# Optimization experiments

Hardware: AMD Instinct MI355X
Metric: run time of the kernel (lower is better)

Reference implementation:

```python
import jax, jax.numpy as jnp
import numpy as np

# dims
M, C, D = 64, 2000, 512          # clients, classes, embed_dim
H = 4                             # num_heads
HD = D // H                       # head_dim = 128
DFF = 2048                        # torch TransformerEncoderLayer default dim_feedforward
NUM_CLASSES = 2000
EPS = 1e-5


def _ln(x, g, b):
    mu = jnp.mean(x, axis=-1, keepdims=True)
    var = jnp.mean(jnp.square(x - mu), axis=-1, keepdims=True)
    return (x - mu) * jax.lax.rsqrt(var + EPS) * g + b


def setup_inputs() -> dict:
    key = jax.random.key(0)
    ks = jax.random.split(key, 16)
    s = 0.02
    return {
        "client_protos": jax.random.normal(ks[0], (M, C, D), jnp.float32),
        "norm_g": jnp.ones((D,), jnp.float32),
        "norm_b": jnp.zeros((D,), jnp.float32),
        "in_proj_w": jax.random.normal(ks[1], (3 * D, D), jnp.float32) * s,
        "in_proj_b": jnp.zeros((3 * D,), jnp.float32),
        "out_proj_w": jax.random.normal(ks[2], (D, D), jnp.float32) * s,
        "out_proj_b": jnp.zeros((D,), jnp.float32),
        "lin1_w": jax.random.normal(ks[3], (DFF, D), jnp.float32) * s,
        "lin1_b": jnp.zeros((DFF,), jnp.float32),
        "lin2_w": jax.random.normal(ks[4], (D, DFF), jnp.float32) * s,
        "lin2_b": jnp.zeros((D,), jnp.float32),
        "norm1_g": jnp.ones((D,), jnp.float32),
        "norm1_b": jnp.zeros((D,), jnp.float32),
        "norm2_g": jnp.ones((D,), jnp.float32),
        "norm2_b": jnp.zeros((D,), jnp.float32),
        "global_query": jax.random.normal(ks[5], (NUM_CLASSES, D), jnp.float32),
        "all_labels": jax.random.randint(ks[6], (C,), 0, NUM_CLASSES, jnp.int32),
        "round_num": 10,
        "client_idx": 0,
    }


def reference(client_protos, norm_g, norm_b, in_proj_w, in_proj_b,
              out_proj_w, out_proj_b, lin1_w, lin1_b, lin2_w, lin2_b,
              norm1_g, norm1_b, norm2_g, norm2_b, global_query,
              all_labels, round_num, client_idx):
    # 1) LayerNorm over all prototypes: (M, C, D)
    x = _ln(client_protos, norm_g, norm_b)
    # 2) Per-class transformer: original loops c in range(C) on (1, M, D).
    #    Batched: treat C as batch -> (C, M, D). Post-norm torch encoder layer.
    x = jnp.transpose(x, (1, 0, 2))  # (C, M, D)
    # self-attention
    qkv = x @ in_proj_w.T + in_proj_b          # (C, M, 3D)
    q, k, v = jnp.split(qkv, 3, axis=-1)
    q = q.reshape(C, M, H, HD)
    k = k.reshape(C, M, H, HD)
    v = v.reshape(C, M, H, HD)
    scores = jnp.einsum('cqhd,ckhd->chqk', q, k) / np.sqrt(HD).astype(np.float32)
    attn = jax.nn.softmax(scores, axis=-1)
    sa = jnp.einsum('chqk,ckhd->cqhd', attn, v).reshape(C, M, D)
    sa = sa @ out_proj_w.T + out_proj_b
    x = _ln(x + sa, norm1_g, norm1_b)
    # feed-forward (relu, dropout = eval no-op)
    ff = jax.nn.relu(x @ lin1_w.T + lin1_b) @ lin2_w.T + lin2_b
    x = _ln(x + ff, norm2_g, norm2_b)           # (C, M, D) == protos_trans^T
    # 3) Cross-attention with per-class global query
    q_all = global_query[all_labels].reshape(C, H, HD)
    kv_all = x.reshape(C, M, H, HD)
    s2 = jnp.einsum('chd,cmhd->chm', q_all, kv_all) / np.sqrt(HD).astype(np.float32)
    w2 = jax.nn.softmax(s2, axis=-1)
    attn_out = jnp.einsum('chm,cmhd->chd', w2, kv_all).reshape(C, D)
    return attn_out
```

## Files before the change

### kernel.cpp

```cpp
#include <hip/hip_runtime.h>

typedef _Float16 f16;
typedef _Float16 half4 __attribute__((ext_vector_type(4)));
typedef _Float16 half8 __attribute__((ext_vector_type(8)));
typedef float f32x4 __attribute__((ext_vector_type(4)));

typedef __attribute__((address_space(1))) void* as1v;
typedef __attribute__((address_space(3))) void* as3v;

#define SCALE 0.08838834764831845f

static __device__ __forceinline__ f32x4 mfma16(half8 a, half8 b, f32x4 c){
  return __builtin_amdgcn_mfma_f32_16x16x32_f16(a, b, c, 0, 0, 0);
}

__global__ __launch_bounds__(256) void k_cvt(const float* __restrict__ src, f16* __restrict__ dst, int n){
  int i = (blockIdx.x * 256 + threadIdx.x) * 8;
  if (i >= n) return;
  float4 a = *(const float4*)(src + i);
  float4 b = *(const float4*)(src + i + 4);
  half8 h;
  h[0] = (f16)a.x; h[1] = (f16)a.y; h[2] = (f16)a.z; h[3] = (f16)a.w;
  h[4] = (f16)b.x; h[5] = (f16)b.y; h[6] = (f16)b.z; h[7] = (f16)b.w;
  *(half8*)(dst + i) = h;
}

__global__ __launch_bounds__(256) void k_ln0(const float* __restrict__ protos,
                                             const float* __restrict__ g,
                                             const float* __restrict__ bb,
                                             f16* __restrict__ xb, int c0){
  const int w = threadIdx.x >> 6, l = threadIdx.x & 63;
  const int q = blockIdx.x * 4 + w;
  const int cl = q >> 6, m = q & 63;
  const float* in = protos + ((size_t)m * 2000 + (size_t)(c0 + cl)) * 512;
  const int d0 = l * 8;
  float4 a = *(const float4*)(in + d0);
  float4 c = *(const float4*)(in + d0 + 4);
  float s  = a.x + a.y + a.z + a.w + c.x + c.y + c.z + c.w;
  float ss = a.x*a.x + a.y*a.y + a.z*a.z + a.w*a.w + c.x*c.x + c.y*c.y + c.z*c.z + c.w*c.w;
#pragma unroll
  for (int msk = 1; msk < 64; msk <<= 1){ s += __shfl_xor(s, msk); ss += __shfl_xor(ss, msk); }
  const float mu = s * (1.f/512.f);
  const float rs = rsqrtf(ss * (1.f/512.f) - mu*mu + 1e-5f);
  float4 g0 = *(const float4*)(g + d0),  g1 = *(const float4*)(g + d0 + 4);
  float4 b0 = *(const float4*)(bb + d0), b1 = *(const float4*)(bb + d0 + 4);
  half8 o;
  o[0] = (f16)((a.x - mu) * rs * g0.x + b0.x);
  o[1] = (f16)((a.y - mu) * rs * g0.y + b0.y);
  o[2] = (f16)((a.z - mu) * rs * g0.z + b0.z);
  o[3] = (f16)((a.w - mu) * rs * g0.w + b0.w);
  o[4] = (f16)((c.x - mu) * rs * g1.x + b1.x);
  o[5] = (f16)((c.y - mu) * rs * g1.y + b1.y);
  o[6] = (f16)((c.z - mu) * rs * g1.z + b1.z);
  o[7] = (f16)((c.w - mu) * rs * g1.w + b1.w);
  *(half8*)(xb + (size_t)q * 512 + d0) = o;
}

__global__ __launch_bounds__(256) void k_resln(const f16* __restrict__ t, const f16* __restrict__ skip,
                                               const float* __restrict__ g, const float* __restrict__ bb,
                                               f16* __restrict__ outp){
  const int w = threadIdx.x >> 6, l = threadIdx.x & 63;
  const size_t q = (size_t)blockIdx.x * 4 + w;
  const int d0 = l * 8;
  half8 tv = *(const half8*)(t + q * 512 + d0);
  half8 sk = *(const half8*)(skip + q * 512 + d0);
  float v0 = (float)tv[0] + (float)sk[0], v1 = (float)tv[1] + (float)sk[1];
  float v2 = (float)tv[2] + (float)sk[2], v3 = (float)tv[3] + (float)sk[3];
  float v4 = (float)tv[4] + (float)sk[4], v5 = (float)tv[5] + (float)sk[5];
  float v6 = (float)tv[6] + (float)sk[6], v7 = (float)tv[7] + (float)sk[7];
  float s  = v0+v1+v2+v3+v4+v5+v6+v7;
  float ss = v0*v0+v1*v1+v2*v2+v3*v3+v4*v4+v5*v5+v6*v6+v7*v7;
#pragma unroll
  for (int msk = 1; msk < 64; msk <<= 1){ s += __shfl_xor(s, msk); ss += __shfl_xor(ss, msk); }
  const float mu = s * (1.f/512.f);
  const float rs = rsqrtf(ss * (1.f/512.f) - mu*mu + 1e-5f);
  float4 g0 = *(const float4*)(g + d0),  g1 = *(const float4*)(g + d0 + 4);
  float4 b0 = *(const float4*)(bb + d0), b1 = *(const float4*)(bb + d0 + 4);
  half8 o;
  o[0] = (f16)((v0 - mu) * rs * g0.x + b0.x);
  o[1] = (f16)((v1 - mu) * rs * g0.y + b0.y);
  o[2] = (f16)((v2 - mu) * rs * g0.z + b0.z);
  o[3] = (f16)((v3 - mu) * rs * g0.w + b0.w);
  o[4] = (f16)((v4 - mu) * rs * g1.x + b1.x);
  o[5] = (f16)((v5 - mu) * rs * g1.y + b1.y);
  o[6] = (f16)((v6 - mu) * rs * g1.z + b1.z);
  o[7] = (f16)((v7 - mu) * rs * g1.w + b1.w);
  *(half8*)(outp + q * 512 + d0) = o;
}

#define GLL(gp, lp) __builtin_amdgcn_global_load_lds((as1v)(void*)(gp), (as3v)(lp), 16, 0, 0)

template<bool RELU>
__global__ __launch_bounds__(256, 2) void k_gemm(const f16* __restrict__ A, const f16* __restrict__ B,
                                                 const float* __restrict__ bias, f16* __restrict__ Cout,
                                                 int N, int K, int gn){
  extern __shared__ char smem_raw[];
  f16* sAB = (f16*)smem_raw;

  const int t = threadIdx.x, w = t >> 6, l = t & 63;
  const int wr = w >> 1, wc = w & 1;

  const int nwg = gridDim.x;
  const int q8 = nwg >> 3, r8 = nwg & 7;
  const int xcd = blockIdx.x & 7, lidx = blockIdx.x >> 3;
  const int swz = (xcd < r8 ? xcd * (q8 + 1) : r8 * (q8 + 1) + (xcd - r8) * q8) + lidx;
  const int tm = swz / gn, tn = swz % gn;
  const size_t row0 = (size_t)tm * 128;
  const int col0 = tn * 256;

  f32x4 acc[4][8];
#pragma unroll
  for (int m = 0; m < 4; ++m)
#pragma unroll
    for (int n = 0; n < 8; ++n) acc[m][n] = (f32x4){0.f,0.f,0.f,0.f};

  const int srcsw = ((t & 3) ^ ((t >> 3) & 3)) * 8;
  const f16* gA = A + (row0 + (size_t)(t >> 2)) * (size_t)K + srcsw;
  const f16* gB = B + ((size_t)col0 + (size_t)(t >> 2)) * (size_t)K + srcsw;
  const int dA = t * 8;
  const int dB = 4096 + t * 8;

  const int ps = (((l >> 4) ^ ((l >> 1) & 3)) << 3);
  const int abase = (wr * 64 + (l & 15)) * 32 + ps;
  const int bbase = 4096 + (wc * 128 + (l & 15)) * 32 + ps;

  const int NT = K >> 5;

  auto stage = [&](int tile){
    f16* buf = sAB + (tile % 3) * 12288;
    const size_t ko = (size_t)tile * 32;
    GLL(gA + ko,                    buf + dA);
    GLL(gA + ko + (size_t)64 * K,   buf + dA + 2048);
    GLL(gB + ko,                    buf + dB);
    GLL(gB + ko + (size_t)64 * K,   buf + dB + 2048);
    GLL(gB + ko + (size_t)128 * K,  buf + dB + 4096);
    GLL(gB + ko + (size_t)192 * K,  buf + dB + 6144);
  };

  stage(0); stage(1);
  asm volatile("s_waitcnt vmcnt(6)" ::: "memory");
  __builtin_amdgcn_s_barrier();

  for (int tk = 0; tk < NT; ++tk){
    const f16* buf = sAB + (tk % 3) * 12288;
    half8 af[4], bf[8];
#pragma unroll
    for (int m = 0; m < 4; ++m) af[m] = *(const half8*)(buf + abase + m * 512);
#pragma unroll
    for (int n = 0; n < 4; ++n) bf[n] = *(const half8*)(buf + bbase + n * 512);
#pragma unroll
    for (int n = 4; n < 8; ++n) bf[n] = *(const half8*)(buf + bbase + n * 512);
    if (tk + 2 < NT) stage(tk + 2);
    asm volatile("s_waitcnt lgkmcnt(4)" ::: "memory");
    __builtin_amdgcn_sched_barrier(0);
    __builtin_amdgcn_s_setprio(1);
#pragma unroll
    for (int m = 0; m < 4; ++m)
#pragma unroll
      for (int n = 0; n < 4; ++n)
        acc[m][n] = mfma16(bf[n], af[m], acc[m][n]);
    __builtin_amdgcn_s_setprio(0);
    asm volatile("s_waitcnt lgkmcnt(0)" ::: "memory");
    __builtin_amdgcn_sched_barrier(0);
    __builtin_amdgcn_s_setprio(1);
#pragma unroll
    for (int m = 0; m < 4; ++m)
#pragma unroll
      for (int n = 4; n < 8; ++n)
        acc[m][n] = mfma16(bf[n], af[m], acc[m][n]);
    __builtin_amdgcn_s_setprio(0);
    if (tk + 2 < NT)      { asm volatile("s_waitcnt vmcnt(6)" ::: "memory"); }
    else if (tk + 1 < NT) { asm volatile("s_waitcnt vmcnt(0)" ::: "memory"); }
    __builtin_amdgcn_s_barrier();
  }

#pragma unroll
  for (int n = 0; n < 8; ++n){
    const int c = col0 + wc * 128 + n * 16 + ((l >> 4) << 2);
    float4 b4 = *(const float4*)(bias + c);
#pragma unroll
    for (int m = 0; m < 4; ++m){
      const size_t r = row0 + (size_t)(wr * 64 + m * 16 + (l & 15));
      float v0 = acc[m][n][0] + b4.x;
      float v1 = acc[m][n][1] + b4.y;
      float v2 = acc[m][n][2] + b4.z;
      float v3 = acc[m][n][3] + b4.w;
      if (RELU){ v0 = fmaxf(v0, 0.f); v1 = fmaxf(v1, 0.f); v2 = fmaxf(v2, 0.f); v3 = fmaxf(v3, 0.f); }
      half4 h; h[0] = (f16)v0; h[1] = (f16)v1; h[2] = (f16)v2; h[3] = (f16)v3;
      *(half4*)&Cout[r * (size_t)N + c] = h;
    }
  }
}

__global__ __launch_bounds__(256) void k_attn(const f16* __restrict__ qkv, f16* __restrict__ sa){
  __shared__ __align__(16) f16 P[4][4096];
  __shared__ __align__(16) f16 VT[4][4096];
  const int cl = blockIdx.x;
  const int h = threadIdx.x >> 6, l = threadIdx.x & 63;
  const f16* base = qkv + (size_t)cl * 64 * 1536;
  const f16* Qp = base + h * 128;
  const f16* Kp = base + 512 + h * 128;
  const f16* Vp = base + 1024 + h * 128;

  f32x4 s[4][4];
#pragma unroll
  for (int x = 0; x < 4; ++x)
#pragma unroll
    for (int y = 0; y < 4; ++y) s[x][y] = (f32x4){0.f,0.f,0.f,0.f};
#pragma unroll
  for (int ks = 0; ks < 4; ++ks){
    half8 aq[4], bk[4];
#pragma unroll
    for (int x = 0; x < 4; ++x)
      aq[x] = *(const half8*)&Qp[(size_t)(x * 16 + (l & 15)) * 1536 + ks * 32 + (l >> 4) * 8];
#pragma unroll
    for (int y = 0; y < 4; ++y)
      bk[y] = *(const half8*)&Kp[(size_t)(y * 16 + (l & 15)) * 1536 + ks * 32 + (l >> 4) * 8];
#pragma unroll
    for (int x = 0; x < 4; ++x)
#pragma unroll
      for (int y = 0; y < 4; ++y)
        s[x][y] = mfma16(aq[x], bk[y], s[x][y]);
  }

  char* Pb = (char*)&P[h][0];
#pragma unroll
  for (int x = 0; x < 4; ++x){
#pragma unroll
    for (int j = 0; j < 4; ++j){
      float e0 = s[x][0][j] * SCALE;
      float e1 = s[x][1][j] * SCALE;
      float e2 = s[x][2][j] * SCALE;
      float e3 = s[x][3][j] * SCALE;
      float mx = fmaxf(fmaxf(e0, e1), fmaxf(e2, e3));
#pragma unroll
      for (int msk = 1; msk < 16; msk <<= 1) mx = fmaxf(mx, __shfl_xor(mx, msk));
      e0 = __expf(e0 - mx); e1 = __expf(e1 - mx); e2 = __expf(e2 - mx); e3 = __expf(e3 - mx);
      float sm = e0 + e1 + e2 + e3;
#pragma unroll
      for (int msk = 1; msk < 16; msk <<= 1) sm += __shfl_xor(sm, msk);
      const float inv = 1.f / sm;
      const int row = x * 16 + (l >> 4) * 4 + j;
      const int rb = row * 128 + (l & 15) * 2;
      const int rsw = (row & 7) << 4;
      *(f16*)(Pb + ((rb     ) ^ rsw)) = (f16)(e0 * inv);
      *(f16*)(Pb + ((rb + 32) ^ rsw)) = (f16)(e1 * inv);
      *(f16*)(Pb + ((rb + 64) ^ rsw)) = (f16)(e2 * inv);
      *(f16*)(Pb + ((rb + 96) ^ rsw)) = (f16)(e3 * inv);
    }
  }

  char* Vb = (char*)&VT[h][0];
#pragma unroll
  for (int dh = 0; dh < 2; ++dh){
#pragma unroll
    for (int it = 0; it < 8; ++it){
      const int chunk = it * 64 + l;
      const int m = chunk >> 3, dc = chunk & 7;
      half8 v = *(const half8*)&Vp[(size_t)m * 1536 + dh * 64 + dc * 8];
#pragma unroll
      for (int jj = 0; jj < 8; ++jj){
        const int dd = dc * 8 + jj;
        *(f16*)(Vb + ((dd * 128 + m * 2) ^ ((dd & 7) << 4))) = v[jj];
      }
    }
    __syncthreads();
#pragma unroll
    for (int x = 0; x < 4; ++x){
      const int ar = x * 16 + (l & 15);
      const int ab = ar * 128, sw = (ar & 7) << 4;
      half8 ap0 = *(const half8*)(Pb + ((ab + (l >> 4) * 16) ^ sw));
      half8 ap1 = *(const half8*)(Pb + ((ab + 64 + (l >> 4) * 16) ^ sw));
#pragma unroll
      for (int dt = 0; dt < 4; ++dt){
        const int vr = dt * 16 + (l & 15);
        const int vb = vr * 128, vsw = (vr & 7) << 4;
        half8 b0 = *(const half8*)(Vb + ((vb + (l >> 4) * 16) ^ vsw));
        half8 b1 = *(const half8*)(Vb + ((vb + 64 + (l >> 4) * 16) ^ vsw));
        f32x4 o = (f32x4){0.f,0.f,0.f,0.f};
        o = mfma16(ap0, b0, o);
        o = mfma16(ap1, b1, o);
#pragma unroll
        for (int j = 0; j < 4; ++j){
          const int mrow = x * 16 + (l >> 4) * 4 + j;
          const int dcol = dh * 64 + dt * 16 + (l & 15);
          sa[((size_t)cl * 64 + mrow) * 512 + h * 128 + dcol] = (f16)o[j];
        }
      }
    }
    __syncthreads();
  }
}

__global__ __launch_bounds__(256) void k_cross(const f16* __restrict__ z, const float* __restrict__ gq,
                                               const int* __restrict__ labels, float* __restrict__ out,
                                               int c0){
  const int cl = blockIdx.x;
  const int h = threadIdx.x >> 6, l = threadIdx.x & 63;
  const int cg = c0 + cl;
  const float* q = gq + (size_t)labels[cg] * 512 + h * 128;
  const f16* zb = z + (size_t)cl * 64 * 512 + h * 128;

  const f16* zr = zb + (size_t)l * 512;
  float s = 0.f;
#pragma unroll
  for (int d = 0; d < 128; d += 8){
    half8 v = *(const half8*)&zr[d];
    float4 q0 = *(const float4*)&q[d];
    float4 q1 = *(const float4*)&q[d + 4];
    s += q0.x*(float)v[0] + q0.y*(float)v[1] + q0.z*(float)v[2] + q0.w*(float)v[3]
       + q1.x*(float)v[4] + q1.y*(float)v[5] + q1.z*(float)v[6] + q1.w*(float)v[7];
  }
  s *= SCALE;
  float mx = s;
#pragma unroll
  for (int msk = 1; msk < 64; msk <<= 1) mx = fmaxf(mx, __shfl_xor(mx, msk));
  float e = __expf(s - mx);
  float sm = e;
#pragma unroll
  for (int msk = 1; msk < 64; msk <<= 1) sm += __shfl_xor(sm, msk);
  const float wgt = e / sm;

  float a0 = 0.f, a1 = 0.f;
  for (int m = 0; m < 64; ++m){
    const float wm = __shfl(wgt, m);
    const f16* zm = zb + (size_t)m * 512 + 2 * l;
    a0 += wm * (float)zm[0];
    a1 += wm * (float)zm[1];
  }
  float2 o; o.x = a0; o.y = a1;
  *(float2*)&out[(size_t)cg * 512 + h * 128 + 2 * l] = o;
}

extern "C" void kernel_launch(void* const* d_in, const int* in_sizes, int n_in,
                              void* d_out, int out_size, void* d_ws, size_t ws_size,
                              hipStream_t stream){
  (void)in_sizes; (void)n_in; (void)out_size;
  const float* protos = (const float*)d_in[0];
  const float* norm_g = (const float*)d_in[1];
  const float* norm_b = (const float*)d_in[2];
  const float* in_w   = (const float*)d_in[3];
  const float* in_b   = (const float*)d_in[4];
  const float* ow     = (const float*)d_in[5];
  const float* ob     = (const float*)d_in[6];
  const float* l1w    = (const float*)d_in[7];
  const float* l1b    = (const float*)d_in[8];
  const float* l2w    = (const float*)d_in[9];
  const float* l2b    = (const float*)d_in[10];
  const float* n1g    = (const float*)d_in[11];
  const float* n1b    = (const float*)d_in[12];
  const float* n2g    = (const float*)d_in[13];
  const float* n2b    = (const float*)d_in[14];
  const float* gq     = (const float*)d_in[15];
  const int*   labels = (const int*)d_in[16];
  float* out = (float*)d_out;

  char* p = (char*)d_ws;
  auto alloc = [&](size_t bytes)->char*{
    char* r = p; p += (bytes + 255) & ~(size_t)255; return r;
  };
  f16* Wq = (f16*)alloc((size_t)1536*512*2);
  f16* Wo = (f16*)alloc((size_t)512*512*2);
  f16* W1 = (f16*)alloc((size_t)2048*512*2);
  f16* W2 = (f16*)alloc((size_t)512*2048*2);
  const size_t fixed = (size_t)(p - (char*)d_ws);

  const size_t per_class = (size_t)64*512*2 + (size_t)64*2048*2 + (size_t)64*512*2 + (size_t)64*512*2;
  long long avail = (long long)ws_size - (long long)fixed - 8192;
  long long cc_max = avail > 0 ? avail / (long long)per_class : 0;
  int Cc = (int)(cc_max > 2000 ? 2000 : cc_max);
  Cc &= ~1;
  if (Cc < 2) Cc = 2;

  f16* xb  = (f16*)alloc((size_t)Cc*64*512*2);
  f16* big = (f16*)alloc((size_t)Cc*64*2048*2);
  f16* sac = (f16*)alloc((size_t)Cc*64*512*2);
  f16* tmp = (f16*)alloc((size_t)Cc*64*512*2);

  k_cvt<<<1536*512/2048, 256, 0, stream>>>(in_w, Wq, 1536*512);
  k_cvt<<<512*512/2048,  256, 0, stream>>>(ow,   Wo, 512*512);
  k_cvt<<<2048*512/2048, 256, 0, stream>>>(l1w,  W1, 2048*512);
  k_cvt<<<2048*512/2048, 256, 0, stream>>>(l2w,  W2, 512*2048);

  const size_t SMEM = 73728;
  for (int c0 = 0; c0 < 2000; c0 += Cc){
    const int cc = (2000 - c0 < Cc) ? (2000 - c0) : Cc;
    const int R = cc * 64;
    const int gm = R / 128;
    k_ln0<<<R/4, 256, 0, stream>>>(protos, norm_g, norm_b, xb, c0);
    k_gemm<false><<<gm*6, 256, SMEM, stream>>>(xb, Wq, in_b, big, 1536, 512, 6);
    k_attn<<<cc, 256, 0, stream>>>(big, sac);
    k_gemm<false><<<gm*2, 256, SMEM, stream>>>(sac, Wo, ob, tmp, 512, 512, 2);
    k_resln<<<R/4, 256, 0, stream>>>(tmp, xb, n1g, n1b, sac);
    k_gemm<true><<<gm*8, 256, SMEM, stream>>>(sac, W1, l1b, big, 2048, 512, 8);
    k_gemm<false><<<gm*2, 256, SMEM, stream>>>(big, W2, l2b, tmp, 512, 2048, 2);
    k_resln<<<R/4, 256, 0, stream>>>(tmp, sac, n2g, n2b, big);
    k_cross<<<cc, 256, 0, stream>>>(big, gq, labels, out, c0);
  }
}
```

Measured before the change: 1.511 ms.

## Enlarge GEMM tile to 256x256 with one block per CU

The GEMM kernel's tile grows from 128x256 to 256x256, so each wave holds an 8x8 grid of MFMA accumulators. The LDS swizzle and staging change to match, and the split LDS-read/MFMA phases become a single load-then-compute phase per k-step. Occupancy drops to one block per CU with a larger LDS footprint. The aim is more arithmetic per LDS/global byte, at the cost of higher register pressure, less latency hiding, and fewer workgroups (R/256 rows) for the 2000*64-row problem.

```diff
diff --git a/kernel.cpp b/kernel.cpp
--- a/kernel.cpp
+++ b/kernel.cpp
@@ -91,11 +91,11 @@
 #define GLL(gp, lp) __builtin_amdgcn_global_load_lds((as1v)(void*)(gp), (as3v)(lp), 16, 0, 0)
 
 template<bool RELU>
-__global__ __launch_bounds__(256, 2) void k_gemm(const f16* __restrict__ A, const f16* __restrict__ B,
+__global__ __launch_bounds__(256, 1) void k_gemm(const f16* __restrict__ A, const f16* __restrict__ B,
                                                  const float* __restrict__ bias, f16* __restrict__ Cout,
                                                  int N, int K, int gn){
   extern __shared__ char smem_raw[];
-  f16* sAB = (f16*)smem_raw;
+  f16* lds = (f16*)smem_raw;
 
   const int t = threadIdx.x, w = t >> 6, l = t & 63;
   const int wr = w >> 1, wc = w & 1;
@@ -105,73 +105,64 @@
   const int xcd = blockIdx.x & 7, lidx = blockIdx.x >> 3;
   const int swz = (xcd < r8 ? xcd * (q8 + 1) : r8 * (q8 + 1) + (xcd - r8) * q8) + lidx;
   const int tm = swz / gn, tn = swz % gn;
-  const size_t row0 = (size_t)tm * 128;
+  const size_t row0 = (size_t)tm * 256;
   const int col0 = tn * 256;
 
-  f32x4 acc[4][8];
-#pragma unroll
-  for (int m = 0; m < 4; ++m)
+  f32x4 acc[8][8];
+#pragma unroll
+  for (int m = 0; m < 8; ++m)
 #pragma unroll
     for (int n = 0; n < 8; ++n) acc[m][n] = (f32x4){0.f,0.f,0.f,0.f};
 
-  const int srcsw = ((t & 3) ^ ((t >> 3) & 3)) * 8;
-  const f16* gA = A + (row0 + (size_t)(t >> 2)) * (size_t)K + srcsw;
-  const f16* gB = B + ((size_t)col0 + (size_t)(t >> 2)) * (size_t)K + srcsw;
-  const int dA = t * 8;
-  const int dB = 4096 + t * 8;
-
-  const int ps = (((l >> 4) ^ ((l >> 1) & 3)) << 3);
-  const int abase = (wr * 64 + (l & 15)) * 32 + ps;
-  const int bbase = 4096 + (wc * 128 + (l & 15)) * 32 + ps;
+  const int srow = t >> 2;
+  const int sslot = (t & 3) ^ ((t >> 2) & 3);
+  const f16* gA = A + (row0 + (size_t)srow) * (size_t)K + sslot * 8;
+  const f16* gB = B + ((size_t)col0 + (size_t)srow) * (size_t)K + sslot * 8;
+  const int dst0 = t * 8;
+
+  const int arow = (l & 15) * 32 + (((l >> 4) ^ (l & 3)) << 3);
+  const int aoff = wr * 128 * 32 + arow;
+  const int boff = 8192 + wc * 128 * 32 + arow;
 
   const int NT = K >> 5;
 
-  auto stage = [&](int tile){
-    f16* buf = sAB + (tile % 3) * 12288;
+  auto stage = [&](int tile, int slot){
+    f16* base = lds + slot * 16384;
     const size_t ko = (size_t)tile * 32;
-    GLL(gA + ko,                    buf + dA);
-    GLL(gA + ko + (size_t)64 * K,   buf + dA + 2048);
-    GLL(gB + ko,                    buf + dB);
-    GLL(gB + ko + (size_t)64 * K,   buf + dB + 2048);
-    GLL(gB + ko + (size_t)128 * K,  buf + dB + 4096);
-    GLL(gB + ko + (size_t)192 * K,  buf + dB + 6144);
+#pragma unroll
+    for (int r = 0; r < 4; ++r)
+      GLL(gA + ko + (size_t)(r * 64) * K, base + r * 2048 + dst0);
+#pragma unroll
+    for (int r = 0; r < 4; ++r)
+      GLL(gB + ko + (size_t)(r * 64) * K, base + 8192 + r * 2048 + dst0);
   };
 
-  stage(0); stage(1);
-  asm volatile("s_waitcnt vmcnt(6)" ::: "memory");
+  stage(0, 0); stage(1, 1);
+  asm volatile("s_waitcnt vmcnt(8)" ::: "memory");
   __builtin_amdgcn_s_barrier();
 
+  int rs = 0, ws = 2;
   for (int tk = 0; tk < NT; ++tk){
-    const f16* buf = sAB + (tk % 3) * 12288;
-    half8 af[4], bf[8];
-#pragma unroll
-    for (int m = 0; m < 4; ++m) af[m] = *(const half8*)(buf + abase + m * 512);
-#pragma unroll
-    for (int n = 0; n < 4; ++n) bf[n] = *(const half8*)(buf + bbase + n * 512);
-#pragma unroll
-    for (int n = 4; n < 8; ++n) bf[n] = *(const half8*)(buf + bbase + n * 512);
-    if (tk + 2 < NT) stage(tk + 2);
-    asm volatile("s_waitcnt lgkmcnt(4)" ::: "memory");
+    if (tk + 2 < NT) stage(tk + 2, ws);
     __builtin_amdgcn_sched_barrier(0);
+    const f16* sb = lds + rs * 16384;
+    half8 af[8], bf[8];
+#pragma unroll
+    for (int m = 0; m < 8; ++m) af[m] = *(const half8*)(sb + aoff + m * 512);
+#pragma unroll
+    for (int n = 0; n < 8; ++n) bf[n] = *(const half8*)(sb + boff + n * 512);
     __builtin_amdgcn_s_setprio(1);
 #pragma unroll
-    for (int m = 0; m < 4; ++m)
-#pragma unroll
-      for (int n = 0; n < 4; ++n)
+    for (int m = 0; m < 8; ++m)
+#pragma unroll
+      for (int n = 0; n < 8; ++n)
         acc[m][n] = mfma16(bf[n], af[m], acc[m][n]);
     __builtin_amdgcn_s_setprio(0);
-    asm volatile("s_waitcnt lgkmcnt(0)" ::: "memory");
-    __builtin_amdgcn_sched_barrier(0);
-    __builtin_amdgcn_s_setprio(1);
-#pragma unroll
-    for (int m = 0; m < 4; ++m)
-#pragma unroll
-      for (int n = 4; n < 8; ++n)
-        acc[m][n] = mfma16(bf[n], af[m], acc[m][n]);
-    __builtin_amdgcn_s_setprio(0);
-    if (tk + 2 < NT)      { asm volatile("s_waitcnt vmcnt(6)" ::: "memory"); }
+    if (tk + 2 < NT)      { asm volatile("s_waitcnt vmcnt(8)" ::: "memory"); }
     else if (tk + 1 < NT) { asm volatile("s_waitcnt vmcnt(0)" ::: "memory"); }
     __builtin_amdgcn_s_barrier();
+    rs = (rs == 2) ? 0 : rs + 1;
+    ws = (ws == 2) ? 0 : ws + 1;
   }
 
 #pragma unroll
@@ -179,8 +170,8 @@
     const int c = col0 + wc * 128 + n * 16 + ((l >> 4) << 2);
     float4 b4 = *(const float4*)(bias + c);
 #pragma unroll
-    for (int m = 0; m < 4; ++m){
-      const size_t r = row0 + (size_t)(wr * 64 + m * 16 + (l & 15));
+    for (int m = 0; m < 8; ++m){
+      const size_t r = row0 + (size_t)(wr * 128 + m * 16 + (l & 15));
       float v0 = acc[m][n][0] + b4.x;
       float v1 = acc[m][n][1] + b4.y;
       float v2 = acc[m][n][2] + b4.z;
@@ -369,8 +360,8 @@
   long long avail = (long long)ws_size - (long long)fixed - 8192;
   long long cc_max = avail > 0 ? avail / (long long)per_class : 0;
   int Cc = (int)(cc_max > 2000 ? 2000 : cc_max);
-  Cc &= ~1;
-  if (Cc < 2) Cc = 2;
+  Cc &= ~3;
+  if (Cc < 4) Cc = 4;
 
   f16* xb  = (f16*)alloc((size_t)Cc*64*512*2);
   f16* big = (f16*)alloc((size_t)Cc*64*2048*2);
@@ -382,11 +373,11 @@
   k_cvt<<<2048*512/2048, 256, 0, stream>>>(l1w,  W1, 2048*512);
   k_cvt<<<2048*512/2048, 256, 0, stream>>>(l2w,  W2, 512*2048);
 
-  const size_t SMEM = 73728;
+  const size_t SMEM = 98304;
   for (int c0 = 0; c0 < 2000; c0 += Cc){
     const int cc = (2000 - c0 < Cc) ? (2000 - c0) : Cc;
     const int R = cc * 64;
-    const int gm = R / 128;
+    const int gm = R / 256;
     k_ln0<<<R/4, 256, 0, stream>>>(protos, norm_g, norm_b, xb, c0);
     k_gemm<false><<<gm*6, 256, SMEM, stream>>>(xb, Wq, in_b, big, 1536, 512, 6);
     k_attn<<<cc, 256, 0, stream>>>(big, sac);
```

Measured after the change: 1.619 ms. 7.1% more time.

## Shrink GEMM tile to 128x128 with static double-buffered LDS

Applied to the files above, without the earlier changes.

Rewrites the GEMM kernel from a 128x256 tile with a 3-stage dynamic-LDS pipeline to a 128x128 tile with a simple 2-buffer static LDS scheme and __syncthreads per k-step. The accumulator count halves and launch bounds rise to 3 blocks per CU, aiming at higher occupancy and more workgroups per GEMM. In exchange it loses the deeper prefetch, the split lgkmcnt waits and setprio scheduling, and it reloads the A tile twice as often.

```diff
diff --git a/kernel.cpp b/kernel.cpp
--- a/kernel.cpp
+++ b/kernel.cpp
@@ -91,11 +91,10 @@
 #define GLL(gp, lp) __builtin_amdgcn_global_load_lds((as1v)(void*)(gp), (as3v)(lp), 16, 0, 0)
 
 template<bool RELU>
-__global__ __launch_bounds__(256, 2) void k_gemm(const f16* __restrict__ A, const f16* __restrict__ B,
+__global__ __launch_bounds__(256, 3) void k_gemm(const f16* __restrict__ A, const f16* __restrict__ B,
                                                  const float* __restrict__ bias, f16* __restrict__ Cout,
                                                  int N, int K, int gn){
-  extern __shared__ char smem_raw[];
-  f16* sAB = (f16*)smem_raw;
+  __shared__ __align__(16) f16 lds[2][8192];
 
   const int t = threadIdx.x, w = t >> 6, l = t & 63;
   const int wr = w >> 1, wc = w & 1;
@@ -106,85 +105,69 @@
   const int swz = (xcd < r8 ? xcd * (q8 + 1) : r8 * (q8 + 1) + (xcd - r8) * q8) + lidx;
   const int tm = swz / gn, tn = swz % gn;
   const size_t row0 = (size_t)tm * 128;
-  const int col0 = tn * 256;
-
-  f32x4 acc[4][8];
+  const int col0 = tn * 128;
+
+  f32x4 acc[4][4];
 #pragma unroll
   for (int m = 0; m < 4; ++m)
 #pragma unroll
-    for (int n = 0; n < 8; ++n) acc[m][n] = (f32x4){0.f,0.f,0.f,0.f};
-
-  const int srcsw = ((t & 3) ^ ((t >> 3) & 3)) * 8;
-  const f16* gA = A + (row0 + (size_t)(t >> 2)) * (size_t)K + srcsw;
-  const f16* gB = B + ((size_t)col0 + (size_t)(t >> 2)) * (size_t)K + srcsw;
-  const int dA = t * 8;
-  const int dB = 4096 + t * 8;
-
-  const int ps = (((l >> 4) ^ ((l >> 1) & 3)) << 3);
-  const int abase = (wr * 64 + (l & 15)) * 32 + ps;
-  const int bbase = 4096 + (wc * 128 + (l & 15)) * 32 + ps;
+    for (int n = 0; n < 4; ++n) acc[m][n] = (f32x4){0.f,0.f,0.f,0.f};
+
+  const int ssl = ((t & 3) ^ ((t >> 3) & 3)) * 8;
+  const f16* gA = A + (row0 + (size_t)(t >> 2)) * (size_t)K + ssl;
+  const f16* gB = B + ((size_t)col0 + (size_t)(t >> 2)) * (size_t)K + ssl;
+  const size_t rows64 = (size_t)64 * K;
+  const int d0 = t * 8;
+
+  const int psl = (((l >> 4) ^ ((l >> 1) & 3)) << 3);
+  const int aoff = (wr * 64 + (l & 15)) * 32 + psl;
+  const int boff = 4096 + (wc * 64 + (l & 15)) * 32 + psl;
 
   const int NT = K >> 5;
 
-  auto stage = [&](int tile){
-    f16* buf = sAB + (tile % 3) * 12288;
-    const size_t ko = (size_t)tile * 32;
-    GLL(gA + ko,                    buf + dA);
-    GLL(gA + ko + (size_t)64 * K,   buf + dA + 2048);
-    GLL(gB + ko,                    buf + dB);
-    GLL(gB + ko + (size_t)64 * K,   buf + dB + 2048);
-    GLL(gB + ko + (size_t)128 * K,  buf + dB + 4096);
-    GLL(gB + ko + (size_t)192 * K,  buf + dB + 6144);
-  };
-
-  stage(0); stage(1);
-  asm volatile("s_waitcnt vmcnt(6)" ::: "memory");
-  __builtin_amdgcn_s_barrier();
+  {
+    f16* bse = &lds[0][0];
+    GLL(gA,          bse + d0);
+    GLL(gA + rows64, bse + 2048 + d0);
+    GLL(gB,          bse + 4096 + d0);
+    GLL(gB + rows64, bse + 6144 + d0);
+  }
+  __syncthreads();
 
   for (int tk = 0; tk < NT; ++tk){
-    const f16* buf = sAB + (tk % 3) * 12288;
-    half8 af[4], bf[8];
-#pragma unroll
-    for (int m = 0; m < 4; ++m) af[m] = *(const half8*)(buf + abase + m * 512);
-#pragma unroll
-    for (int n = 0; n < 4; ++n) bf[n] = *(const half8*)(buf + bbase + n * 512);
-#pragma unroll
-    for (int n = 4; n < 8; ++n) bf[n] = *(const half8*)(buf + bbase + n * 512);
-    if (tk + 2 < NT) stage(tk + 2);
-    asm volatile("s_waitcnt lgkmcnt(4)" ::: "memory");
-    __builtin_amdgcn_sched_barrier(0);
-    __builtin_amdgcn_s_setprio(1);
-#pragma unroll
-    for (int m = 0; m < 4; ++m)
-#pragma unroll
-      for (int n = 0; n < 4; ++n)
-        acc[m][n] = mfma16(bf[n], af[m], acc[m][n]);
-    __builtin_amdgcn_s_setprio(0);
-    asm volatile("s_waitcnt lgkmcnt(0)" ::: "memory");
-    __builtin_amdgcn_sched_barrier(0);
-    __builtin_amdgcn_s_setprio(1);
-#pragma unroll
-    for (int m = 0; m < 4; ++m)
-#pragma unroll
-      for (int n = 4; n < 8; ++n)
-        acc[m][n] = mfma16(bf[n], af[m], acc[m][n]);
-    __builtin_amdgcn_s_setprio(0);
-    if (tk + 2 < NT)      { asm volatile("s_waitcnt vmcnt(6)" ::: "memory"); }
-    else if (tk + 1 < NT) { asm volatile("s_waitcnt vmcnt(0)" ::: "memory"); }
-    __builtin_amdgcn_s_barrier();
-  }
-
-#pragma unroll
-  for (int n = 0; n < 8; ++n){
-    const int c = col0 + wc * 128 + n * 16 + ((l >> 4) << 2);
+    if (tk + 1 < NT){
+      f16* bse = &lds[(tk + 1) & 1][0];
+      const size_t ko = (size_t)(tk + 1) * 32;
+      GLL(gA + ko,          bse + d0);
+      GLL(gA + ko + rows64, bse + 2048 + d0);
+      GLL(gB + ko,          bse + 4096 + d0);
+      GLL(gB + ko + rows64, bse + 6144 + d0);
+    }
+    const f16* sb = &lds[tk & 1][0];
+    half8 af[4], bf[4];
+#pragma unroll
+    for (int x = 0; x < 4; ++x) af[x] = *(const half8*)(sb + aoff + x * 512);
+#pragma unroll
+    for (int y = 0; y < 4; ++y) bf[y] = *(const half8*)(sb + boff + y * 512);
+#pragma unroll
+    for (int x = 0; x < 4; ++x)
+#pragma unroll
+      for (int y = 0; y < 4; ++y)
+        acc[x][y] = mfma16(bf[y], af[x], acc[x][y]);
+    __syncthreads();
+  }
+
+#pragma unroll
+  for (int y = 0; y < 4; ++y){
+    const int c = col0 + wc * 64 + y * 16 + ((l >> 4) << 2);
     float4 b4 = *(const float4*)(bias + c);
 #pragma unroll
-    for (int m = 0; m < 4; ++m){
-      const size_t r = row0 + (size_t)(wr * 64 + m * 16 + (l & 15));
-      float v0 = acc[m][n][0] + b4.x;
-      float v1 = acc[m][n][1] + b4.y;
-      float v2 = acc[m][n][2] + b4.z;
-      float v3 = acc[m][n][3] + b4.w;
+    for (int x = 0; x < 4; ++x){
+      const size_t r = row0 + (size_t)(wr * 64 + x * 16 + (l & 15));
+      float v0 = acc[x][y][0] + b4.x;
+      float v1 = acc[x][y][1] + b4.y;
+      float v2 = acc[x][y][2] + b4.z;
+      float v3 = acc[x][y][3] + b4.w;
       if (RELU){ v0 = fmaxf(v0, 0.f); v1 = fmaxf(v1, 0.f); v2 = fmaxf(v2, 0.f); v3 = fmaxf(v3, 0.f); }
       half4 h; h[0] = (f16)v0; h[1] = (f16)v1; h[2] = (f16)v2; h[3] = (f16)v3;
       *(half4*)&Cout[r * (size_t)N + c] = h;
@@ -382,18 +365,17 @@
   k_cvt<<<2048*512/2048, 256, 0, stream>>>(l1w,  W1, 2048*512);
   k_cvt<<<2048*512/2048, 256, 0, stream>>>(l2w,  W2, 512*2048);
 
-  const size_t SMEM = 73728;
   for (int c0 = 0; c0 < 2000; c0 += Cc){
     const int cc = (2000 - c0 < Cc) ? (2000 - c0) : Cc;
     const int R = cc * 64;
     const int gm = R / 128;
     k_ln0<<<R/4, 256, 0, stream>>>(protos, norm_g, norm_b, xb, c0);
-    k_gemm<false><<<gm*6, 256, SMEM, stream>>>(xb, Wq, in_b, big, 1536, 512, 6);
+    k_gemm<false><<<gm*12, 256, 0, stream>>>(xb, Wq, in_b, big, 1536, 512, 12);
     k_attn<<<cc, 256, 0, stream>>>(big, sac);
-    k_gemm<false><<<gm*2, 256, SMEM, stream>>>(sac, Wo, ob, tmp, 512, 512, 2);
+    k_gemm<false><<<gm*4, 256, 0, stream>>>(sac, Wo, ob, tmp, 512, 512, 4);
     k_resln<<<R/4, 256, 0, stream>>>(tmp, xb, n1g, n1b, sac);
-    k_gemm<true><<<gm*8, 256, SMEM, stream>>>(sac, W1, l1b, big, 2048, 512, 8);
-    k_gemm<false><<<gm*2, 256, SMEM, stream>>>(big, W2, l2b, tmp, 512, 2048, 2);
+    k_gemm<true><<<gm*16, 256, 0, stream>>>(sac, W1, l1b, big, 2048, 512, 16);
+    k_gemm<false><<<gm*4, 256, 0, stream>>>(big, W2, l2b, tmp, 512, 2048, 4);
     k_resln<<<R/4, 256, 0, stream>>>(tmp, sac, n2g, n2b, big);
     k_cross<<<cc, 256, 0, stream>>>(big, gq, labels, out, c0);
   }
```

Result: slower. 1.608 ms (+6.4%).
